# Performance work log

Measured on AMD Instinct MI355X. Metric: run time of the kernel, lower is better.

Reference implementation:

```python
import jax, jax.numpy as jnp
import numpy as np

FILTER_LENGTHS = (2, 4)  # from module: self.filter_length = [2, 4]


def _get_conv(signal, b, h, l, d_k, conv, w):
    # signal: [b, h*d_k, l] (raw reshape of [b,h,l,d_k], matching torch .reshape)
    f = max(FILTER_LENGTHS)
    pad = f // 2
    padded = jnp.pad(signal, ((0, 0), (0, 0), (pad, pad)))  # [b, d, l+f]
    # unfold(-1, f, 1)[:, :, :l, :] -> sliding windows, keep first l
    idx = jnp.arange(l)[:, None] + jnp.arange(f)[None, :]  # [l, f]
    seq = padded[:, :, idx]  # [b, d, l, f]
    # dynamic filter-length selection: w_f = filter_lengths * w, pick argmax
    f_s = jnp.asarray(FILTER_LENGTHS, dtype=signal.dtype)
    ind = jnp.argmax(f_s * w)
    chosen_len = jnp.asarray(FILTER_LENGTHS)[ind]
    mask = (jnp.arange(f) < chosen_len).astype(signal.dtype)  # [f]
    seq = seq * mask  # broadcast over [b, d, l, f]
    # depthwise-ish conv via einsum, then raw reshape (b, l, h*d_k) -> (b, h, l, d_k)
    out = jnp.einsum('bdlf,dof->blo', seq, conv)
    return out.reshape(b, h, l, d_k)


def reference(Q, K, V, attn_mask, conv_q, conv_k, w):
    b, h, l, d_k = Q.shape
    Qc = _get_conv(Q.reshape(b, h * d_k, l), b, h, l, d_k, conv_q, w) + Q
    Kc = _get_conv(K.reshape(b, h * d_k, l), b, h, l, d_k, conv_k, w) + K
    scores = jnp.einsum('bhqd,bhkd->bhqk', Qc, Kc) / np.sqrt(d_k).astype(Q.dtype)
    attn = jax.nn.softmax(scores, axis=-1)
    context = jnp.einsum('bhqk,bhkd->bhqd', attn, V)
    return context, attn


def setup_inputs() -> dict:
    key = jax.random.key(0)
    ks = jax.random.split(key, 6)
    b, h, l, d_k = 4, 8, 2048, 64
    d = h * d_k
    f = max(FILTER_LENGTHS)
    return {
        'Q': jax.random.normal(ks[0], (b, h, l, d_k), dtype=jnp.float32),
        'K': jax.random.normal(ks[1], (b, h, l, d_k), dtype=jnp.float32),
        'V': jax.random.normal(ks[2], (b, h, l, d_k), dtype=jnp.float32),
        'attn_mask': jnp.zeros((b, 1, l, l), dtype=bool),  # unused by forward
        'conv_q': jax.random.normal(ks[3], (d, d, f), dtype=jnp.float32),
        'conv_k': jax.random.normal(ks[4], (d, d, f), dtype=jnp.float32),
        'w': jax.random.normal(ks[5], (2,), dtype=jnp.float32),
    }
```

## Files before the change

### kernel.cpp

```cpp
#include <hip/hip_runtime.h>

typedef _Float16 f16;
typedef _Float16 f16x8 __attribute__((ext_vector_type(8)));
typedef float f32x16 __attribute__((ext_vector_type(16)));

#define MFMA32(A, B, C) __builtin_amdgcn_mfma_f32_32x32x16_f16(A, B, C, 0, 0, 0)

constexpr int Bb = 4, Hh = 8, Ll = 2048, Dk = 64, Dm = 512, BH = 32;

constexpr size_t NWF = (size_t)16 * 128 * 64 * 8;
constexpr size_t NAF = (size_t)Bb * 64 * 128 * 64 * 8;
constexpr size_t NFF = (size_t)BH * 64 * 4 * 64 * 8;
constexpr size_t NVF = (size_t)BH * 2 * 128 * 64 * 8;

constexpr size_t OFF_WF = 256;
constexpr size_t OFF_AF = OFF_WF + 4 * NWF * sizeof(f16);
constexpr size_t OFF_FF = OFF_AF + 4 * NAF * sizeof(f16);
constexpr size_t OFF_VF = OFF_FF + 4 * NFF * sizeof(f16);

#define QSCALE 0.1803368801111204f

__global__ void kprep_w(const float* __restrict__ convq, const float* __restrict__ convk,
                        const float* __restrict__ w, int* __restrict__ flag,
                        f16* __restrict__ wfhq, f16* __restrict__ wflq,
                        f16* __restrict__ wfhk, f16* __restrict__ wflk) {
    const int len = (4.f * w[1] > 2.f * w[0]) ? 4 : 2;
    if (blockIdx.x == 0 && blockIdx.y == 0 && threadIdx.x == 0) *flag = len;
    int tid = blockIdx.x * 256 + threadIdx.x;
    int o = tid & 511;
    const float* conv = blockIdx.y ? convk : convq;
    f16* dh = blockIdx.y ? wfhk : wfhq;
    f16* dl = blockIdx.y ? wflk : wflq;
    const float4 v = *(const float4*)(conv + (size_t)tid * 4);
    float vv[4] = {v.x, v.y, v.z, v.w};
    int c = tid >> 9, ob = o >> 5;
#pragma unroll
    for (int f = 0; f < 4; ++f) {
        float x = (f < len) ? vv[f] : 0.f;
        f16 hi = (f16)x;
        f16 lo = (f16)(x - (float)hi);
        int k = (f << 9) + c;
        size_t idx = (((size_t)ob * 128 + (k >> 4)) * 64 + ((k >> 3) & 1) * 32 + (o & 31)) * 8 + (k & 7);
        dh[idx] = hi; dl[idx] = lo;
    }
}

__global__ void kprep_a(const float* __restrict__ Q, const float* __restrict__ K,
                        const int* __restrict__ flag,
                        f16* __restrict__ afhq, f16* __restrict__ aflq,
                        f16* __restrict__ afhk, f16* __restrict__ aflk) {
    __shared__ float tile[64][36];
    int tensor = blockIdx.z, b = blockIdx.y;
    int tb = blockIdx.x >> 5, k16g = blockIdx.x & 31;
    int f = k16g >> 3;
    if (f >= *flag) return;
    int c0 = (k16g * 64) & 511;
    const float* S = (tensor ? K : Q) + (size_t)b * Dm * Ll;
    int tid = threadIdx.x;
    int t0 = tb * 32;
#pragma unroll
    for (int i = 0; i < 9; ++i) {
        int e = i * 256 + tid;
        int row = e / 36, col = e - row * 36;
        int t = t0 - 2 + col;
        tile[row][col] = (t >= 0 && t < Ll) ? S[(size_t)(c0 + row) * Ll + t] : 0.f;
    }
    __syncthreads();
    int sub = tid >> 6, lane = tid & 63;
    int k16 = k16g * 4 + sub;
    int khalf = lane >> 5, lane31 = lane & 31;
    f16x8 hv, lv;
#pragma unroll
    for (int j = 0; j < 8; ++j) {
        int cl = sub * 16 + khalf * 8 + j;
        float x = tile[cl][lane31 + f];
        f16 hi = (f16)x;
        hv[j] = hi; lv[j] = (f16)(x - (float)hi);
    }
    f16* dh = tensor ? afhk : afhq;
    f16* dl = tensor ? aflk : aflq;
    size_t idx = ((((size_t)b * 64 + tb) * 128 + k16) * 64 + lane) * 8;
    *(f16x8*)(dh + idx) = hv;
    *(f16x8*)(dl + idx) = lv;
}

__global__ void kprep_v(const float* __restrict__ V, f16* __restrict__ vf) {
    int bh = blockIdx.y, l0 = blockIdx.x * 128;
    int tid = threadIdx.x;
    const float* src = V + (size_t)bh * Ll * Dk;
#pragma unroll
    for (int s = 0; s < 4; ++s) {
        int g = s * 4 + (tid >> 6);
        int lane = tid & 63;
        int l16s = g >> 1, db = g & 1;
        int khalf = lane >> 5, lane31 = lane & 31;
        int d = db * 32 + lane31;
        f16x8 out;
#pragma unroll
        for (int j = 0; j < 8; ++j) {
            int l = l0 + l16s * 16 + khalf * 8 + j;
            out[j] = (f16)src[(size_t)l * Dk + d];
        }
        size_t idx = ((((size_t)bh * 2 + db) * 128 + (l0 >> 4) + l16s) * 64 + lane) * 8;
        *(f16x8*)(vf + idx) = out;
    }
}

__global__ __launch_bounds__(256, 4) void kconv(
    const float* __restrict__ Q, const float* __restrict__ K, const int* __restrict__ flag,
    const f16* __restrict__ afhq, const f16* __restrict__ aflq,
    const f16* __restrict__ afhk, const f16* __restrict__ aflk,
    const f16* __restrict__ wfhq, const f16* __restrict__ wflq,
    const f16* __restrict__ wfhk, const f16* __restrict__ wflk,
    f16* __restrict__ ffhq, f16* __restrict__ fflq,
    f16* __restrict__ ffhk, f16* __restrict__ fflk) {
    int id = blockIdx.x;
    int xcd = id & 7, oTile = (id >> 3) & 3, gidx = id >> 5;
    int g = gidx * 8 + xcd;
    int tt = g & 31, b = (g >> 5) & 3, tensor = (g >> 7) & 1;
    int wave = threadIdx.x >> 6, lane = threadIdx.x & 63;
    int wn = wave & 1, wm = wave >> 1;
    int lane31 = lane & 31, khalf = lane >> 5;
    const f16* ah = (tensor ? afhk : afhq) + ((size_t)(b * 64 + tt * 2 + wm) * 128) * 512;
    const f16* al = (tensor ? aflk : aflq) + ((size_t)(b * 64 + tt * 2 + wm) * 128) * 512;
    const f16* bhp = (tensor ? wfhk : wfhq) + ((size_t)(oTile * 4 + wn * 2) * 128) * 512;
    const f16* blp = (tensor ? wflk : wflq) + ((size_t)(oTile * 4 + wn * 2) * 128) * 512;
    const float* src = (tensor ? K : Q) + (size_t)b * Hh * Ll * Dk;
    f16* dh = (tensor ? ffhk : ffhq);
    f16* dl = (tensor ? fflk : fflq);
    const float scale = tensor ? 1.f : QSCALE;
    const int klen16 = (*flag) << 5;

    f32x16 acc[2];
#pragma unroll
    for (int j = 0; j < 2; ++j)
#pragma unroll
        for (int r = 0; r < 16; ++r) acc[j][r] = 0.f;

    f16x8 Aah, Aal, Abh[2], Abl[2];
    f16x8 Bah, Bal, Bbh[2], Bbl[2];
    const size_t lo8 = (size_t)lane * 8;

    Aah = *(const f16x8*)(ah + lo8);
    Aal = *(const f16x8*)(al + lo8);
    Abh[0] = *(const f16x8*)(bhp + lo8);
    Abl[0] = *(const f16x8*)(blp + lo8);
    Abh[1] = *(const f16x8*)(bhp + 128 * 512 + lo8);
    Abl[1] = *(const f16x8*)(blp + 128 * 512 + lo8);

    for (int k16 = 0; k16 < klen16; k16 += 2) {
        {
            int kn = k16 + 1 < klen16 ? k16 + 1 : k16;
            size_t o = (size_t)kn * 512 + lo8;
            Bah = *(const f16x8*)(ah + o);
            Bal = *(const f16x8*)(al + o);
            Bbh[0] = *(const f16x8*)(bhp + o);
            Bbl[0] = *(const f16x8*)(blp + o);
            Bbh[1] = *(const f16x8*)(bhp + 128 * 512 + o);
            Bbl[1] = *(const f16x8*)(blp + 128 * 512 + o);
        }
#pragma unroll
        for (int j = 0; j < 2; ++j) {
            acc[j] = MFMA32(Aah, Abh[j], acc[j]);
            acc[j] = MFMA32(Aah, Abl[j], acc[j]);
            acc[j] = MFMA32(Aal, Abh[j], acc[j]);
        }
        {
            int kn = k16 + 2 < klen16 ? k16 + 2 : klen16 - 1;
            size_t o = (size_t)kn * 512 + lo8;
            Aah = *(const f16x8*)(ah + o);
            Aal = *(const f16x8*)(al + o);
            Abh[0] = *(const f16x8*)(bhp + o);
            Abl[0] = *(const f16x8*)(blp + o);
            Abh[1] = *(const f16x8*)(bhp + 128 * 512 + o);
            Abl[1] = *(const f16x8*)(blp + 128 * 512 + o);
        }
#pragma unroll
        for (int j = 0; j < 2; ++j) {
            acc[j] = MFMA32(Bah, Bbh[j], acc[j]);
            acc[j] = MFMA32(Bah, Bbl[j], acc[j]);
            acc[j] = MFMA32(Bal, Bbh[j], acc[j]);
        }
    }
#pragma unroll
    for (int j = 0; j < 2; ++j)
#pragma unroll
        for (int r = 0; r < 16; ++r) {
            int trow = tt * 64 + wm * 32 + (r & 3) + ((r >> 2) << 3) + (khalf << 2);
            int ocol = oTile * 128 + wn * 64 + j * 32 + lane31;
            int h = trow >> 8;
            int l = ((trow & 255) << 3) + (ocol >> 6);
            int d = ocol & 63;
            float v2 = (acc[j][r] + src[((size_t)h * Ll + l) * Dk + d]) * scale;
            f16 hi = (f16)v2;
            f16 lo = (f16)(v2 - (float)hi);
            size_t idx = ((((size_t)(b * 8 + h) * 64 + (l >> 5)) * 4 + (d >> 4)) * 64
                          + ((d >> 3) & 1) * 32 + (l & 31)) * 8 + (d & 7);
            dh[idx] = hi; dl[idx] = lo;
        }
}

__global__ __launch_bounds__(256, 3) void kattn(
    const f16* __restrict__ qfh, const f16* __restrict__ qfl,
    const f16* __restrict__ kfh, const f16* __restrict__ kfl,
    const f16* __restrict__ vf,
    float* __restrict__ ctx_out, float* __restrict__ attn_out) {
    __shared__ float combuf[2][32][64];
    __shared__ __align__(16) f16 ptile[4][32][40];
    int id = blockIdx.x;
    int bh = (id & 7) * 4 + (id >> 8);
    int qt = (id >> 3) & 31;
    int wave = threadIdx.x >> 6, lane = threadIdx.x & 63;
    int qg = wave >> 1, kg = wave & 1;
    int lane31 = lane & 31, khalf = lane >> 5;
    int q0 = qt * 64 + qg * 32;

    f16x8 a_h[4], a_l[4];
    {
        size_t qb = ((size_t)bh * 64 + qt * 2 + qg) * 4;
#pragma unroll
        for (int ks = 0; ks < 4; ++ks) {
            a_h[ks] = *(const f16x8*)(qfh + ((qb + ks) * 64 + lane) * 8);
            a_l[ks] = *(const f16x8*)(qfl + ((qb + ks) * 64 + lane) * 8);
        }
    }
    const f16* kbh = kfh + (size_t)bh * 131072;
    const f16* kbl = kfl + (size_t)bh * 131072;
    const int ch0 = kg * 32, ch1 = ch0 + 32;

    float m[16], s[16];
#pragma unroll
    for (int r = 0; r < 16; ++r) { m[r] = -3.0e38f; s[r] = 0.f; }

    for (int ch = ch0; ch < ch1; ++ch) {
        f32x16 acc;
#pragma unroll
        for (int r = 0; r < 16; ++r) acc[r] = 0.f;
        size_t kb = (size_t)ch * 2048 + lane * 8;
#pragma unroll
        for (int ks = 0; ks < 4; ++ks) {
            f16x8 kh8 = *(const f16x8*)(kbh + kb + ks * 512);
            f16x8 kl8 = *(const f16x8*)(kbl + kb + ks * 512);
            acc = MFMA32(a_h[ks], kh8, acc);
            acc = MFMA32(a_h[ks], kl8, acc);
            acc = MFMA32(a_l[ks], kh8, acc);
        }
#pragma unroll
        for (int r = 0; r < 16; ++r) {
            float v = acc[r];
            float d = v - m[r];
            float e = exp2f(-fabsf(d));
            bool gt = d > 0.f;
            s[r] = gt ? __fmaf_rn(s[r], e, 1.f) : (s[r] + e);
            m[r] = gt ? v : m[r];
        }
    }
#pragma unroll
    for (int r = 0; r < 16; ++r) {
        float mm = m[r], ss = s[r];
#pragma unroll
        for (int off = 1; off < 32; off <<= 1) {
            float mo = __shfl_xor(mm, off, 64);
            float so = __shfl_xor(ss, off, 64);
            float mn = fmaxf(mm, mo);
            ss = ss * exp2f(mm - mn) + so * exp2f(mo - mn);
            mm = mn;
        }
        m[r] = mm; s[r] = ss;
    }
    if (kg == 1) {
#pragma unroll
        for (int r = 0; r < 16; ++r) {
            combuf[qg][r][lane] = m[r];
            combuf[qg][16 + r][lane] = s[r];
        }
    }
    __syncthreads();
    if (kg == 0) {
#pragma unroll
        for (int r = 0; r < 16; ++r) {
            float m1 = combuf[qg][r][lane];
            float s1 = combuf[qg][16 + r][lane];
            float mn = fmaxf(m[r], m1);
            float ss = s[r] * exp2f(m[r] - mn) + s1 * exp2f(m1 - mn);
            m[r] = mn; s[r] = 1.f / ss;
            combuf[qg][r][lane] = mn;
            combuf[qg][16 + r][lane] = s[r];
        }
    }
    __syncthreads();
    if (kg == 1) {
#pragma unroll
        for (int r = 0; r < 16; ++r) {
            m[r] = combuf[qg][r][lane];
            s[r] = combuf[qg][16 + r][lane];
        }
    }

    f32x16 ctx[2];
#pragma unroll
    for (int n = 0; n < 2; ++n)
#pragma unroll
        for (int r = 0; r < 16; ++r) ctx[n][r] = 0.f;

    const size_t rowbase = ((size_t)bh * Ll + q0 + lane31) * Ll;

    for (int ch = ch0; ch < ch1; ++ch) {
        f32x16 acc;
#pragma unroll
        for (int r = 0; r < 16; ++r) acc[r] = 0.f;
        size_t kb = (size_t)ch * 2048 + lane * 8;
#pragma unroll
        for (int ks = 0; ks < 4; ++ks) {
            f16x8 kh8 = *(const f16x8*)(kbh + kb + ks * 512);
            f16x8 kl8 = *(const f16x8*)(kbl + kb + ks * 512);
            acc = MFMA32(a_h[ks], kh8, acc);
            acc = MFMA32(a_h[ks], kl8, acc);
            acc = MFMA32(a_l[ks], kh8, acc);
        }
#pragma unroll
        for (int r = 0; r < 16; ++r) {
            float p = exp2f(acc[r] - m[r]) * s[r];
            int row = (r & 3) + ((r >> 2) << 3) + (khalf << 2);
            ptile[wave][row][lane31] = (f16)p;
        }
        __asm__ volatile("s_waitcnt lgkmcnt(0)" ::: "memory");
#pragma unroll
        for (int ks2 = 0; ks2 < 2; ++ks2) {
            f16x8 pa = *(const f16x8*)&ptile[wave][lane31][ks2 * 16 + khalf * 8];
            float* dst = attn_out + rowbase + ch * 32 + ks2 * 16 + khalf * 8;
            float4 v0 = {(float)pa[0], (float)pa[1], (float)pa[2], (float)pa[3]};
            float4 v1 = {(float)pa[4], (float)pa[5], (float)pa[6], (float)pa[7]};
            *(float4*)dst = v0;
            *(float4*)(dst + 4) = v1;
#pragma unroll
            for (int n = 0; n < 2; ++n) {
                size_t off = ((((size_t)bh * 2 + n) * 128 + ch * 2 + ks2) * 64 + lane) * 8;
                f16x8 vb = *(const f16x8*)(vf + off);
                ctx[n] = MFMA32(pa, vb, ctx[n]);
            }
        }
    }
    __syncthreads();
    if (kg == 1) {
#pragma unroll
        for (int n = 0; n < 2; ++n)
#pragma unroll
            for (int r = 0; r < 16; ++r) combuf[qg][n * 16 + r][lane] = ctx[n][r];
    }
    __syncthreads();
    if (kg == 0) {
#pragma unroll
        for (int n = 0; n < 2; ++n)
#pragma unroll
            for (int r = 0; r < 16; ++r) {
                float v = ctx[n][r] + combuf[qg][n * 16 + r][lane];
                int row = (r & 3) + ((r >> 2) << 3) + (khalf << 2);
                ctx_out[((size_t)bh * Ll + q0 + row) * Dk + n * 32 + lane31] = v;
            }
    }
}

extern "C" void kernel_launch(void* const* d_in, const int* in_sizes, int n_in,
                              void* d_out, int out_size, void* d_ws, size_t ws_size,
                              hipStream_t stream) {
    const float* Q = (const float*)d_in[0];
    const float* K = (const float*)d_in[1];
    const float* V = (const float*)d_in[2];
    const float* convq = (const float*)d_in[4];
    const float* convk = (const float*)d_in[5];
    const float* w = (const float*)d_in[6];

    char* ws = (char*)d_ws;
    int* flag = (int*)ws;
    f16* wfhq = (f16*)(ws + OFF_WF);
    f16* wflq = wfhq + NWF;
    f16* wfhk = wflq + NWF;
    f16* wflk = wfhk + NWF;
    f16* afhq = (f16*)(ws + OFF_AF);
    f16* aflq = afhq + NAF;
    f16* afhk = aflq + NAF;
    f16* aflk = afhk + NAF;
    f16* ffhq = (f16*)(ws + OFF_FF);
    f16* fflq = ffhq + NFF;
    f16* ffhk = fflq + NFF;
    f16* fflk = ffhk + NFF;
    f16* vf = (f16*)(ws + OFF_VF);

    float* ctx_out = (float*)d_out;
    float* attn_out = ctx_out + (size_t)BH * Ll * Dk;

    kprep_w<<<dim3(1024, 2), 256, 0, stream>>>(convq, convk, w, flag, wfhq, wflq, wfhk, wflk);
    kprep_v<<<dim3(16, 32), 256, 0, stream>>>(V, vf);
    kprep_a<<<dim3(2048, 4, 2), 256, 0, stream>>>(Q, K, flag, afhq, aflq, afhk, aflk);
    kconv<<<dim3(1024), 256, 0, stream>>>(Q, K, flag, afhq, aflq, afhk, aflk,
                                          wfhq, wflq, wfhk, wflk, ffhq, fflq, ffhk, fflk);
    kattn<<<dim3(1024), 256, 0, stream>>>(ffhq, fflq, ffhk, fflk, vf, ctx_out, attn_out);
}
```

Measured before the change: 1.075 ms.

## Software-pipeline K/V loads and batch attn-probability stores through wider LDS tile

Double-buffers the K fragment loads in both passes and prefetches V alongside the next K, so global loads for chunk n+1 overlap the MFMA and softmax work of chunk n. The probability tile in LDS is widened to hold four 32-column chunks. The attention matrix is then written as full 128-float row segments with nontemporal float4 stores instead of scattered 8-float pieces per chunk. This is meant to hide load latency and coalesce the large attn_out write stream, at the cost of more registers (which may hurt occupancy at launch bounds 3) and more LDS per block.

```diff
diff --git a/kernel.cpp b/kernel.cpp
--- a/kernel.cpp
+++ b/kernel.cpp
@@ -1,7 +1,9 @@
 #include <hip/hip_runtime.h>
 
 typedef _Float16 f16;
+typedef _Float16 f16x4 __attribute__((ext_vector_type(4)));
 typedef _Float16 f16x8 __attribute__((ext_vector_type(8)));
+typedef float f32x4 __attribute__((ext_vector_type(4)));
 typedef float f32x16 __attribute__((ext_vector_type(16)));
 
 #define MFMA32(A, B, C) __builtin_amdgcn_mfma_f32_32x32x16_f16(A, B, C, 0, 0, 0)
@@ -200,13 +202,34 @@
         }
 }
 
+#define LOADK(DST, CH) do { size_t kb_ = (size_t)(CH) * 2048 + lane * 8;            \
+    _Pragma("unroll") for (int ks_ = 0; ks_ < 4; ++ks_) {                           \
+        DST[2 * ks_]     = *(const f16x8*)(kbh + kb_ + ks_ * 512);                  \
+        DST[2 * ks_ + 1] = *(const f16x8*)(kbl + kb_ + ks_ * 512); } } while (0)
+
+#define QKM(SRC, ACC) do { _Pragma("unroll") for (int ks_ = 0; ks_ < 4; ++ks_) {    \
+        ACC = MFMA32(a_h[ks_], SRC[2 * ks_], ACC);                                  \
+        ACC = MFMA32(a_h[ks_], SRC[2 * ks_ + 1], ACC);                              \
+        ACC = MFMA32(a_l[ks_], SRC[2 * ks_], ACC); } } while (0)
+
+#define SMUPD(ACC) do { _Pragma("unroll") for (int r_ = 0; r_ < 16; ++r_) {         \
+        float v_ = ACC[r_]; float d_ = v_ - m[r_]; float e_ = exp2f(-fabsf(d_));    \
+        bool gt_ = d_ > 0.f;                                                        \
+        s[r_] = gt_ ? __fmaf_rn(s[r_], e_, 1.f) : (s[r_] + e_);                     \
+        m[r_] = gt_ ? v_ : m[r_]; } } while (0)
+
+#define LOADV(DST, CH) do { _Pragma("unroll") for (int q_ = 0; q_ < 4; ++q_) {      \
+        int n_ = q_ >> 1, ks2_ = q_ & 1;                                            \
+        size_t off_ = ((((size_t)bh * 2 + n_) * 128 + (CH) * 2 + ks2_) * 64 + lane) * 8; \
+        DST[q_] = *(const f16x8*)(vf + off_); } } while (0)
+
 __global__ __launch_bounds__(256, 3) void kattn(
     const f16* __restrict__ qfh, const f16* __restrict__ qfl,
     const f16* __restrict__ kfh, const f16* __restrict__ kfl,
     const f16* __restrict__ vf,
     float* __restrict__ ctx_out, float* __restrict__ attn_out) {
     __shared__ float combuf[2][32][64];
-    __shared__ __align__(16) f16 ptile[4][32][40];
+    __shared__ __align__(16) f16 sbuf[4][32][136];
     int id = blockIdx.x;
     int bh = (id & 7) * 4 + (id >> 8);
     int qt = (id >> 3) & 31;
@@ -232,27 +255,25 @@
 #pragma unroll
     for (int r = 0; r < 16; ++r) { m[r] = -3.0e38f; s[r] = 0.f; }
 
-    for (int ch = ch0; ch < ch1; ++ch) {
-        f32x16 acc;
-#pragma unroll
-        for (int r = 0; r < 16; ++r) acc[r] = 0.f;
-        size_t kb = (size_t)ch * 2048 + lane * 8;
-#pragma unroll
-        for (int ks = 0; ks < 4; ++ks) {
-            f16x8 kh8 = *(const f16x8*)(kbh + kb + ks * 512);
-            f16x8 kl8 = *(const f16x8*)(kbl + kb + ks * 512);
-            acc = MFMA32(a_h[ks], kh8, acc);
-            acc = MFMA32(a_h[ks], kl8, acc);
-            acc = MFMA32(a_l[ks], kh8, acc);
-        }
-#pragma unroll
-        for (int r = 0; r < 16; ++r) {
-            float v = acc[r];
-            float d = v - m[r];
-            float e = exp2f(-fabsf(d));
-            bool gt = d > 0.f;
-            s[r] = gt ? __fmaf_rn(s[r], e, 1.f) : (s[r] + e);
-            m[r] = gt ? v : m[r];
+    {
+        f16x8 KA[8], KB[8];
+        LOADK(KA, ch0);
+        for (int ch = ch0; ch < ch1; ch += 2) {
+            LOADK(KB, ch + 1);
+            f32x16 acc;
+#pragma unroll
+            for (int r = 0; r < 16; ++r) acc[r] = 0.f;
+            QKM(KA, acc);
+            SMUPD(acc);
+            {
+                int chn = (ch + 2 < ch1) ? ch + 2 : ch;
+                LOADK(KA, chn);
+            }
+            f32x16 acc2;
+#pragma unroll
+            for (int r = 0; r < 16; ++r) acc2[r] = 0.f;
+            QKM(KB, acc2);
+            SMUPD(acc2);
         }
     }
 #pragma unroll
@@ -303,41 +324,44 @@
 #pragma unroll
         for (int r = 0; r < 16; ++r) ctx[n][r] = 0.f;
 
-    const size_t rowbase = ((size_t)bh * Ll + q0 + lane31) * Ll;
-
-    for (int ch = ch0; ch < ch1; ++ch) {
-        f32x16 acc;
-#pragma unroll
-        for (int r = 0; r < 16; ++r) acc[r] = 0.f;
-        size_t kb = (size_t)ch * 2048 + lane * 8;
-#pragma unroll
-        for (int ks = 0; ks < 4; ++ks) {
-            f16x8 kh8 = *(const f16x8*)(kbh + kb + ks * 512);
-            f16x8 kl8 = *(const f16x8*)(kbl + kb + ks * 512);
-            acc = MFMA32(a_h[ks], kh8, acc);
-            acc = MFMA32(a_h[ks], kl8, acc);
-            acc = MFMA32(a_l[ks], kh8, acc);
-        }
-#pragma unroll
-        for (int r = 0; r < 16; ++r) {
-            float p = exp2f(acc[r] - m[r]) * s[r];
-            int row = (r & 3) + ((r >> 2) << 3) + (khalf << 2);
-            ptile[wave][row][lane31] = (f16)p;
-        }
-        __asm__ volatile("s_waitcnt lgkmcnt(0)" ::: "memory");
-#pragma unroll
-        for (int ks2 = 0; ks2 < 2; ++ks2) {
-            f16x8 pa = *(const f16x8*)&ptile[wave][lane31][ks2 * 16 + khalf * 8];
-            float* dst = attn_out + rowbase + ch * 32 + ks2 * 16 + khalf * 8;
-            float4 v0 = {(float)pa[0], (float)pa[1], (float)pa[2], (float)pa[3]};
-            float4 v1 = {(float)pa[4], (float)pa[5], (float)pa[6], (float)pa[7]};
-            *(float4*)dst = v0;
-            *(float4*)(dst + 4) = v1;
-#pragma unroll
-            for (int n = 0; n < 2; ++n) {
-                size_t off = ((((size_t)bh * 2 + n) * 128 + ch * 2 + ks2) * 64 + lane) * 8;
-                f16x8 vb = *(const f16x8*)(vf + off);
-                ctx[n] = MFMA32(pa, vb, ctx[n]);
+    const size_t rowbase = ((size_t)bh * Ll + q0) * Ll;
+
+    {
+        f16x8 KV[8], VV[4];
+        LOADK(KV, ch0);
+        LOADV(VV, ch0);
+        for (int chb = ch0; chb < ch1; chb += 4) {
+#pragma unroll
+            for (int i = 0; i < 4; ++i) {
+                int ch = chb + i;
+                f32x16 acc;
+#pragma unroll
+                for (int r = 0; r < 16; ++r) acc[r] = 0.f;
+                QKM(KV, acc);
+                int chn = (ch + 1 < ch1) ? ch + 1 : ch;
+                LOADK(KV, chn);
+#pragma unroll
+                for (int r = 0; r < 16; ++r) {
+                    float p = exp2f(acc[r] - m[r]) * s[r];
+                    int row = (r & 3) + ((r >> 2) << 3) + (khalf << 2);
+                    sbuf[wave][row][i * 32 + lane31] = (f16)p;
+                }
+                __asm__ volatile("s_waitcnt lgkmcnt(0)" ::: "memory");
+#pragma unroll
+                for (int ks2 = 0; ks2 < 2; ++ks2) {
+                    f16x8 pa = *(const f16x8*)&sbuf[wave][lane31][i * 32 + ks2 * 16 + khalf * 8];
+                    ctx[0] = MFMA32(pa, VV[ks2], ctx[0]);
+                    ctx[1] = MFMA32(pa, VV[2 + ks2], ctx[1]);
+                }
+                LOADV(VV, chn);
+            }
+#pragma unroll
+            for (int ri = 0; ri < 16; ++ri) {
+                int row = ri * 2 + khalf;
+                f16x4 pv = *(const f16x4*)&sbuf[wave][row][lane31 * 4];
+                f32x4 o = {(float)pv[0], (float)pv[1], (float)pv[2], (float)pv[3]};
+                __builtin_nontemporal_store(
+                    o, (f32x4*)(attn_out + rowbase + (size_t)row * Ll + chb * 32 + lane31 * 4));
             }
         }
     }
```

Result: slower. 1.133 ms (+5.4%).
